# Kernel tuning notes

Hardware: AMD Instinct MI355X
Metric: run time of the kernel (lower is better)

Reference implementation:

```python
import jax, jax.numpy as jnp
import numpy as np

N_HEADS = 16
D_EMBED = 1024
D_CROSS = 768
D_HEAD = D_EMBED // N_HEADS
B, S = 4, 2048


def setup_inputs() -> dict:
    key = jax.random.key(0)
    ks = jax.random.split(key, 10)
    sq = lambda k, shp, fan: jax.random.normal(k, shp, jnp.float32) / np.sqrt(fan)
    return {
        "x": jax.random.normal(ks[0], (B, S, D_EMBED), jnp.float32),
        "y": jax.random.normal(ks[1], (B, S, D_CROSS), jnp.float32),
        "Wq": sq(ks[2], (D_EMBED, D_EMBED), D_EMBED),
        "bq": jnp.zeros((D_EMBED,), jnp.float32),
        "Wk": sq(ks[3], (D_CROSS, D_EMBED), D_CROSS),
        "bk": jnp.zeros((D_EMBED,), jnp.float32),
        "Wv": sq(ks[4], (D_CROSS, D_EMBED), D_CROSS),
        "bv": jnp.zeros((D_EMBED,), jnp.float32),
        "Wo": sq(ks[5], (D_EMBED, D_EMBED), D_EMBED),
        "bo": jnp.zeros((D_EMBED,), jnp.float32),
    }


def reference(x, y, Wq, bq, Wk, bk, Wv, bv, Wo, bo):
    b, s, _ = y.shape
    q = x @ Wq + bq  # [b, s, d_embed]
    k = y @ Wk + bk
    v = y @ Wv + bv
    # [b, h, s, d_head]
    q = q.reshape(b, s, N_HEADS, D_HEAD).transpose(0, 2, 1, 3)
    k = k.reshape(b, s, N_HEADS, D_HEAD).transpose(0, 2, 1, 3)
    v = v.reshape(b, s, N_HEADS, D_HEAD).transpose(0, 2, 1, 3)
    scale = 1.0 / np.sqrt(D_HEAD).astype(np.float32)
    scores = jnp.einsum("bhqd,bhkd->bhqk", q, k) * scale
    weights = jax.nn.softmax(scores, axis=-1)
    out = jnp.einsum("bhqk,bhkd->bhqd", weights, v)
    out = out.transpose(0, 2, 1, 3).reshape(x.shape)
    return out @ Wo + bo
```

## Files before the change

kernel.cpp:

```cpp
#include <hip/hip_runtime.h>

#define NHEADS 16
#define DEMBED 1024
#define DCROSS 768
#define DHEAD  64
#define BATCH  4
#define SLEN   2048
#define MROWS  (BATCH * SLEN)

using bf16   = __bf16;
using bf16x8 = __attribute__((ext_vector_type(8))) __bf16;
using bf16x4 = __attribute__((ext_vector_type(4))) __bf16;
using bf16x2 = __attribute__((ext_vector_type(2))) __bf16;
using f32x4  = __attribute__((ext_vector_type(4))) float;
using f32x16 = __attribute__((ext_vector_type(16))) float;

__device__ __forceinline__ f32x4 mfma_bf16(bf16x8 a, bf16x8 b, f32x4 c) {
    return __builtin_amdgcn_mfma_f32_16x16x32_bf16(a, b, c, 0, 0, 0);
}
__device__ __forceinline__ f32x16 mfma32(bf16x8 a, bf16x8 b, f32x16 c) {
    return __builtin_amdgcn_mfma_f32_32x32x16_bf16(a, b, c, 0, 0, 0);
}

__device__ __forceinline__ void gl2lds16(const void* g, void* l) {
    __builtin_amdgcn_global_load_lds(
        (const __attribute__((address_space(1))) void*)g,
        (__attribute__((address_space(3))) void*)l, 16, 0, 0);
}

struct PrepArgs {
    const float* wsrc[4]; bf16* wdst[4]; int wK[4];
    const float *x, *y; bf16 *xb, *yb;
};
#define NTRB 4096
__global__ void prep_all(PrepArgs a) {
    const int bid = blockIdx.x;
    const int tid = threadIdx.x;
    if (bid < NTRB) {
        __shared__ float tile[32][33];
        const int which = bid >> 10, rem = bid & 1023;
        const int K = a.wK[which], N = DEMBED;
        const int n0 = (rem & 31) * 32, k0 = (rem >> 5) * 32;
        if (k0 >= K) return;
        const float* W = a.wsrc[which];
        bf16* Wt = a.wdst[which];
        const int tx = tid & 31, ty = tid >> 5;
#pragma unroll
        for (int i = 0; i < 32; i += 8)
            tile[ty + i][tx] = W[(size_t)(k0 + ty + i) * N + n0 + tx];
        __syncthreads();
#pragma unroll
        for (int i = 0; i < 32; i += 8)
            Wt[(size_t)(n0 + ty + i) * K + k0 + tx] = (bf16)tile[tx][ty + i];
    } else {
        const int n4x = MROWS * DEMBED / 4;
        const int n4y = MROWS * DCROSS / 4;
        int i = (bid - NTRB) * 256 + tid;
        const float* src; bf16* dst; int j;
        if (i < n4x) { src = a.x; dst = a.xb; j = i; }
        else { j = i - n4x; if (j >= n4y) return; src = a.y; dst = a.yb; }
        float4 v = ((const float4*)src)[j];
        bf16x4 o = { (bf16)v.x, (bf16)v.y, (bf16)v.z, (bf16)v.w };
        ((bf16x4*)dst)[j] = o;
    }
}

struct QkvArgs {
    const bf16 *xb, *yb, *Wqt, *Wkt, *Wvt;
    const float *bq, *bk, *bv;
    bf16 *Qb, *Kb, *Vt;
    float qscale;
};
__global__ __launch_bounds__(256, 3) void gemm_qkv(QkvArgs a) {
    __shared__ bf16 As[128 * 64];
    __shared__ bf16 Bs[128 * 64];
    const int id = blockIdx.x;
    const int cls = id >> 9;
    const bf16 *A, *Bt;
    const float* bias;
    int K, m0, n0;
    if (cls == 0) { int t = id;        m0 = (t >> 3) * 128; n0 = (t & 7) * 128;
                    A = a.xb;  Bt = a.Wqt; bias = a.bq; K = DEMBED; }
    else if (cls == 1) { int t = id - 512;  m0 = (t >> 3) * 128; n0 = (t & 7) * 128;
                    A = a.yb;  Bt = a.Wkt; bias = a.bk; K = DCROSS; }
    else { int t = id - 1024; m0 = (t >> 6) * 128; n0 = (t & 63) * 128;
                    A = a.Wvt; Bt = a.yb;  bias = a.bv; K = DCROSS; }

    const int tid  = threadIdx.x;
    const int wave = tid >> 6, lane = tid & 63;
    const int quad = lane >> 4, l15 = lane & 15;
    const int wr = wave >> 1, wc = wave & 1;

    const int srow = wave * 8 + (lane >> 3);
    const int scol = ((lane & 7) ^ (lane >> 3)) * 8;
    char* ldsA0 = (char*)As + wave * 1024;
    char* ldsB0 = (char*)Bs + wave * 1024;
    const bf16* gA0 = A + (size_t)(m0 + srow) * K + scol;
    const bf16* gB0 = Bt + (size_t)(n0 + srow) * K + scol;

    const int sw = l15 & 7;

    f32x4 acc[4][4] = {};

    for (int kt = 0; kt < K; kt += 64) {
        __syncthreads();
#pragma unroll
        for (int c = 0; c < 4; c++)
            gl2lds16(gA0 + (size_t)c * 32 * K + kt, ldsA0 + c * 4096);
#pragma unroll
        for (int c = 0; c < 4; c++)
            gl2lds16(gB0 + (size_t)c * 32 * K + kt, ldsB0 + c * 4096);
        __syncthreads();

#pragma unroll
        for (int kg = 0; kg < 2; kg++) {
            bf16x8 af[4], bfr[4];
#pragma unroll
            for (int i = 0; i < 4; i++)
                af[i] = *(const bf16x8*)((const char*)As +
                         (wr * 64 + i * 16 + l15) * 128 + (((kg * 4 + quad) ^ sw) * 16));
#pragma unroll
            for (int i = 0; i < 4; i++)
                bfr[i] = *(const bf16x8*)((const char*)Bs +
                         (wc * 64 + i * 16 + l15) * 128 + (((kg * 4 + quad) ^ sw) * 16));
#pragma unroll
            for (int fr = 0; fr < 4; fr++)
#pragma unroll
                for (int fc = 0; fc < 4; fc++)
                    acc[fr][fc] = mfma_bf16(af[fr], bfr[fc], acc[fr][fc]);
        }
    }

    if (cls < 2) {
        bf16* Cout = (cls == 0) ? a.Qb : a.Kb;
        const float alpha = (cls == 0) ? a.qscale : 1.0f;
#pragma unroll
        for (int fr = 0; fr < 4; fr++) {
            int row = m0 + wr * 64 + fr * 16 + quad * 4;
#pragma unroll
            for (int fc = 0; fc < 4; fc++) {
                int col = n0 + wc * 64 + fc * 16 + l15;
                float bv = bias[col];
#pragma unroll
                for (int r = 0; r < 4; r++)
                    Cout[(size_t)(row + r) * DEMBED + col] =
                        (bf16)((acc[fr][fc][r] + bv) * alpha);
            }
        }
    } else {
        const int b = n0 >> 11;
        const size_t bbase = (size_t)b * DEMBED * SLEN;
#pragma unroll
        for (int fr = 0; fr < 4; fr++) {
            int row = m0 + wr * 64 + fr * 16 + quad * 4;
#pragma unroll
            for (int fc = 0; fc < 4; fc++) {
                int col = n0 + wc * 64 + fc * 16 + l15;
                int s = col & (SLEN - 1);
#pragma unroll
                for (int r = 0; r < 4; r++)
                    a.Vt[bbase + (size_t)(row + r) * SLEN + s] =
                        (bf16)(acc[fr][fc][r] + bias[row + r]);
            }
        }
    }
}

__global__ __launch_bounds__(256, 3) void gemm_o(const bf16* __restrict__ A,
                                                 const bf16* __restrict__ Bt,
                                                 const float* __restrict__ bias,
                                                 float* __restrict__ Cout) {
    const int K = DEMBED, N = DEMBED;
    __shared__ bf16 As[128 * 64];
    __shared__ bf16 Bs[128 * 64];
    const int tid  = threadIdx.x;
    const int wave = tid >> 6, lane = tid & 63;
    const int quad = lane >> 4, l15 = lane & 15;
    const int m0 = blockIdx.x * 128, n0 = blockIdx.y * 128;
    const int wr = wave >> 1, wc = wave & 1;

    const int srow = wave * 8 + (lane >> 3);
    const int scol = ((lane & 7) ^ (lane >> 3)) * 8;
    char* ldsA0 = (char*)As + wave * 1024;
    char* ldsB0 = (char*)Bs + wave * 1024;
    const bf16* gA0 = A + (size_t)(m0 + srow) * K + scol;
    const bf16* gB0 = Bt + (size_t)(n0 + srow) * K + scol;

    const int sw = l15 & 7;

    f32x4 acc[4][4] = {};

    for (int kt = 0; kt < K; kt += 64) {
        __syncthreads();
#pragma unroll
        for (int c = 0; c < 4; c++)
            gl2lds16(gA0 + (size_t)c * 32 * K + kt, ldsA0 + c * 4096);
#pragma unroll
        for (int c = 0; c < 4; c++)
            gl2lds16(gB0 + (size_t)c * 32 * K + kt, ldsB0 + c * 4096);
        __syncthreads();

#pragma unroll
        for (int kg = 0; kg < 2; kg++) {
            bf16x8 af[4], bfr[4];
#pragma unroll
            for (int i = 0; i < 4; i++)
                af[i] = *(const bf16x8*)((const char*)As +
                         (wr * 64 + i * 16 + l15) * 128 + (((kg * 4 + quad) ^ sw) * 16));
#pragma unroll
            for (int i = 0; i < 4; i++)
                bfr[i] = *(const bf16x8*)((const char*)Bs +
                         (wc * 64 + i * 16 + l15) * 128 + (((kg * 4 + quad) ^ sw) * 16));
#pragma unroll
            for (int fr = 0; fr < 4; fr++)
#pragma unroll
                for (int fc = 0; fc < 4; fc++)
                    acc[fr][fc] = mfma_bf16(af[fr], bfr[fc], acc[fr][fc]);
        }
    }

#pragma unroll
    for (int fr = 0; fr < 4; fr++) {
        int row = m0 + wr * 64 + fr * 16 + quad * 4;
#pragma unroll
        for (int fc = 0; fc < 4; fc++) {
            int col = n0 + wc * 64 + fc * 16 + l15;
            float bv = bias[col];
#pragma unroll
            for (int r = 0; r < 4; r++)
                Cout[(size_t)(row + r) * N + col] = acc[fr][fc][r] + bv;
        }
    }
}

__global__ __launch_bounds__(256, 4) void attn(const bf16* __restrict__ Q,
                                               const bf16* __restrict__ K,
                                               const bf16* __restrict__ Vt,
                                               bf16* __restrict__ O) {
    __shared__ bf16 KsA[2][64 * 64];
    __shared__ bf16 VsA[2][64 * 64];

    const int tid  = threadIdx.x;
    const int wave = tid >> 6, lane = tid & 63;
    const int l31  = lane & 31, H = lane >> 5;
    const int bh = blockIdx.x, b = bh >> 4, h = bh & 15;
    const size_t rowbase = (size_t)b * SLEN;
    const int qb = blockIdx.y * 128 + wave * 32;
    const int hc = h * DHEAD;

    bf16x8 qf[4];
#pragma unroll
    for (int ks = 0; ks < 4; ks++)
        qf[ks] = *(const bf16x8*)(Q + (rowbase + qb + l31) * DEMBED
                                  + hc + ks * 16 + H * 8);

    f32x16 o[2] = {};
    float lsv = 0.0f;

    const bf16* Kbase = K + rowbase * DEMBED + hc;
    const bf16* Vbase = Vt + (size_t)bh * DHEAD * SLEN;

    const int xcol = (((tid & 7) ^ ((tid >> 3) & 7)) * 8);
    const bf16* gK = Kbase + (size_t)(tid >> 3) * DEMBED + xcol;
    const bf16* gV = Vbase + (size_t)(tid >> 3) * SLEN + xcol;

    const int swz = l31 & 7;

    const int off = (bh * 5 + blockIdx.y * 11) & 31;

    auto STAGE = [&](int buf, int kb) {
        char* lk = (char*)KsA + buf * 8192 + wave * 1024;
        char* lv = (char*)VsA + buf * 8192 + wave * 1024;
        gl2lds16(gK + (size_t)kb * DEMBED, lk);
        gl2lds16(gK + (size_t)(kb + 32) * DEMBED, lk + 32 * 128);
        gl2lds16(gV + kb, lv);
        gl2lds16(gV + 32 * SLEN + kb, lv + 32 * 128);
    };

    STAGE(0, off << 6);
    __syncthreads();

    int cur = 0;
    for (int ss = 0; ss < 32; ++ss) {
        if (ss < 31) STAGE(cur ^ 1, ((ss + off + 1) & 31) << 6);

        const char* Kbuf = (const char*)KsA + cur * 8192;
        const char* Vbuf = (const char*)VsA + cur * 8192;

        f32x16 s0 = {}, s1 = {};
#pragma unroll
        for (int ks = 0; ks < 4; ks++) {
            bf16x8 kf0 = *(const bf16x8*)(Kbuf + l31 * 128
                          + (((2 * ks + H) ^ swz) * 16));
            bf16x8 kf1 = *(const bf16x8*)(Kbuf + (32 + l31) * 128
                          + (((2 * ks + H) ^ swz) * 16));
            s0 = mfma32(kf0, qf[ks], s0);
            s1 = mfma32(kf1, qf[ks], s1);
        }

        int c0[8], c1[8];
#pragma unroll
        for (int t = 0; t < 8; t++) {
            float a0 = __builtin_amdgcn_exp2f(s0[2 * t]);
            float a1 = __builtin_amdgcn_exp2f(s0[2 * t + 1]);
            float b0 = __builtin_amdgcn_exp2f(s1[2 * t]);
            float b1 = __builtin_amdgcn_exp2f(s1[2 * t + 1]);
            lsv += (a0 + a1) + (b0 + b1);
            union { bf16x2 h; int i; } p0, p1;
            p0.h[0] = (bf16)a0; p0.h[1] = (bf16)a1;
            p1.h[0] = (bf16)b0; p1.h[1] = (bf16)b1;
            c0[t] = p0.i;
            c1[t] = p1.i;
        }

#pragma unroll
        for (int ks = 0; ks < 4; ks++) {
            const int* cc = (ks < 2) ? c0 : c1;
            const int ksl = ks & 1;
            auto w0 = __builtin_amdgcn_permlane32_swap(cc[4 * ksl + 0],
                                                       cc[4 * ksl + 2], false, false);
            auto w1 = __builtin_amdgcn_permlane32_swap(cc[4 * ksl + 1],
                                                       cc[4 * ksl + 3], false, false);
            union { int i[4]; bf16x8 v; } ap;
            ap.i[0] = w0[0]; ap.i[1] = w1[0]; ap.i[2] = w0[1]; ap.i[3] = w1[1];
#pragma unroll
            for (int dg = 0; dg < 2; dg++) {
                bf16x8 vf = *(const bf16x8*)(Vbuf + (dg * 32 + l31) * 128
                              + (((2 * ks + H) ^ swz) * 16));
                o[dg] = mfma32(ap.v, vf, o[dg]);
            }
        }

        __syncthreads();
        cur ^= 1;
    }

    lsv += __shfl_xor(lsv, 32);
    float inv = 1.0f / lsv;
#pragma unroll
    for (int r = 0; r < 16; r++) {
        const int ql = (r & 3) + 8 * (r >> 2) + 4 * H;
        float iv = __shfl(inv, ql);
#pragma unroll
        for (int dg = 0; dg < 2; dg++)
            O[(rowbase + qb + ql) * DEMBED + hc + dg * 32 + l31] =
                (bf16)(o[dg][r] * iv);
    }
}

extern "C" void kernel_launch(void* const* d_in, const int* in_sizes, int n_in,
                              void* d_out, int out_size, void* d_ws, size_t ws_size,
                              hipStream_t stream) {
    const float* x  = (const float*)d_in[0];
    const float* y  = (const float*)d_in[1];
    const float* Wq = (const float*)d_in[2];
    const float* bq = (const float*)d_in[3];
    const float* Wk = (const float*)d_in[4];
    const float* bk = (const float*)d_in[5];
    const float* Wv = (const float*)d_in[6];
    const float* bv = (const float*)d_in[7];
    const float* Wo = (const float*)d_in[8];
    const float* bo = (const float*)d_in[9];
    float* out = (float*)d_out;

    char* ws = (char*)d_ws;
    size_t off = 0;
    auto alloc = [&](size_t bytes) {
        void* p = ws + off;
        off += (bytes + 255) & ~(size_t)255;
        return p;
    };
    bf16* xb  = (bf16*)alloc((size_t)MROWS * DEMBED * 2);
    bf16* yb  = (bf16*)alloc((size_t)MROWS * DCROSS * 2);
    bf16* Wqt = (bf16*)alloc((size_t)DEMBED * DEMBED * 2);
    bf16* Wkt = (bf16*)alloc((size_t)DEMBED * DCROSS * 2);
    bf16* Wvt = (bf16*)alloc((size_t)DEMBED * DCROSS * 2);
    bf16* Wot = (bf16*)alloc((size_t)DEMBED * DEMBED * 2);
    bf16* Qb  = (bf16*)alloc((size_t)MROWS * DEMBED * 2);
    bf16* Kb  = (bf16*)alloc((size_t)MROWS * DEMBED * 2);
    bf16* Vtb = (bf16*)alloc((size_t)MROWS * DEMBED * 2);
    bf16* Ab  = (bf16*)alloc((size_t)MROWS * DEMBED * 2);
    if (off > ws_size) return;

    {
        PrepArgs a;
        a.wsrc[0] = Wq; a.wdst[0] = Wqt; a.wK[0] = DEMBED;
        a.wsrc[1] = Wk; a.wdst[1] = Wkt; a.wK[1] = DCROSS;
        a.wsrc[2] = Wv; a.wdst[2] = Wvt; a.wK[2] = DCROSS;
        a.wsrc[3] = Wo; a.wdst[3] = Wot; a.wK[3] = DEMBED;
        a.x = x; a.y = y; a.xb = xb; a.yb = yb;
        int ncvt = (MROWS * DEMBED / 4 + MROWS * DCROSS / 4 + 255) / 256;
        prep_all<<<NTRB + ncvt, 256, 0, stream>>>(a);
    }

    {
        QkvArgs a;
        a.xb = xb; a.yb = yb; a.Wqt = Wqt; a.Wkt = Wkt; a.Wvt = Wvt;
        a.bq = bq; a.bk = bk; a.bv = bv;
        a.Qb = Qb; a.Kb = Kb; a.Vt = Vtb;
        a.qscale = 0.125f * 1.4426950408889634f;
        gemm_qkv<<<1536, 256, 0, stream>>>(a);
    }

    attn<<<dim3(BATCH * NHEADS, SLEN / 128), 256, 0, stream>>>(Qb, Kb, Vtb, Ab);

    gemm_o<<<dim3(MROWS / 128, DEMBED / 128), 256, 0, stream>>>(Ab, Wot, bo, out);
}
```

Baseline: 282.6 us.

## Fuse K and V projections into one block sharing the y tile

```diff
diff --git a/kernel.cpp b/kernel.cpp
--- a/kernel.cpp
+++ b/kernel.cpp
@@ -71,21 +71,12 @@
     bf16 *Qb, *Kb, *Vt;
     float qscale;
 };
-__global__ __launch_bounds__(256, 3) void gemm_qkv(QkvArgs a) {
-    __shared__ bf16 As[128 * 64];
-    __shared__ bf16 Bs[128 * 64];
+__global__ __launch_bounds__(256, 2) void gemm_qkv(QkvArgs a) {
+    __shared__ bf16 Ys[128 * 64];
+    __shared__ bf16 Ks[128 * 64];
+    __shared__ bf16 Vs[128 * 64];
+
     const int id = blockIdx.x;
-    const int cls = id >> 9;
-    const bf16 *A, *Bt;
-    const float* bias;
-    int K, m0, n0;
-    if (cls == 0) { int t = id;        m0 = (t >> 3) * 128; n0 = (t & 7) * 128;
-                    A = a.xb;  Bt = a.Wqt; bias = a.bq; K = DEMBED; }
-    else if (cls == 1) { int t = id - 512;  m0 = (t >> 3) * 128; n0 = (t & 7) * 128;
-                    A = a.yb;  Bt = a.Wkt; bias = a.bk; K = DCROSS; }
-    else { int t = id - 1024; m0 = (t >> 6) * 128; n0 = (t & 63) * 128;
-                    A = a.Wvt; Bt = a.yb;  bias = a.bv; K = DCROSS; }
-
     const int tid  = threadIdx.x;
     const int wave = tid >> 6, lane = tid & 63;
     const int quad = lane >> 4, l15 = lane & 15;
@@ -93,74 +84,144 @@
 
     const int srow = wave * 8 + (lane >> 3);
     const int scol = ((lane & 7) ^ (lane >> 3)) * 8;
-    char* ldsA0 = (char*)As + wave * 1024;
-    char* ldsB0 = (char*)Bs + wave * 1024;
-    const bf16* gA0 = A + (size_t)(m0 + srow) * K + scol;
-    const bf16* gB0 = Bt + (size_t)(n0 + srow) * K + scol;
-
+    char* ldsY0 = (char*)Ys + wave * 1024;
+    char* ldsK0 = (char*)Ks + wave * 1024;
+    char* ldsV0 = (char*)Vs + wave * 1024;
     const int sw = l15 & 7;
 
-    f32x4 acc[4][4] = {};
-
-    for (int kt = 0; kt < K; kt += 64) {
-        __syncthreads();
-#pragma unroll
-        for (int c = 0; c < 4; c++)
-            gl2lds16(gA0 + (size_t)c * 32 * K + kt, ldsA0 + c * 4096);
-#pragma unroll
-        for (int c = 0; c < 4; c++)
-            gl2lds16(gB0 + (size_t)c * 32 * K + kt, ldsB0 + c * 4096);
-        __syncthreads();
-
-#pragma unroll
-        for (int kg = 0; kg < 2; kg++) {
-            bf16x8 af[4], bfr[4];
-#pragma unroll
-            for (int i = 0; i < 4; i++)
-                af[i] = *(const bf16x8*)((const char*)As +
-                         (wr * 64 + i * 16 + l15) * 128 + (((kg * 4 + quad) ^ sw) * 16));
-#pragma unroll
-            for (int i = 0; i < 4; i++)
-                bfr[i] = *(const bf16x8*)((const char*)Bs +
-                         (wc * 64 + i * 16 + l15) * 128 + (((kg * 4 + quad) ^ sw) * 16));
-#pragma unroll
-            for (int fr = 0; fr < 4; fr++)
-#pragma unroll
-                for (int fc = 0; fc < 4; fc++)
-                    acc[fr][fc] = mfma_bf16(af[fr], bfr[fc], acc[fr][fc]);
-        }
-    }
-
-    if (cls < 2) {
-        bf16* Cout = (cls == 0) ? a.Qb : a.Kb;
-        const float alpha = (cls == 0) ? a.qscale : 1.0f;
+    if (id < 512) {
+        const int t = id;
+        const int m0 = (t >> 3) * 128, n0 = (t & 7) * 128;
+        const int K = DEMBED;
+        const bf16* gA0 = a.xb + (size_t)(m0 + srow) * K + scol;
+        const bf16* gB0 = a.Wqt + (size_t)(n0 + srow) * K + scol;
+
+        f32x4 acc[4][4] = {};
+
+        for (int kt = 0; kt < K; kt += 64) {
+            __syncthreads();
+#pragma unroll
+            for (int c = 0; c < 4; c++)
+                gl2lds16(gA0 + (size_t)c * 32 * K + kt, ldsY0 + c * 4096);
+#pragma unroll
+            for (int c = 0; c < 4; c++)
+                gl2lds16(gB0 + (size_t)c * 32 * K + kt, ldsK0 + c * 4096);
+            __syncthreads();
+
+#pragma unroll
+            for (int kg = 0; kg < 2; kg++) {
+                bf16x8 af[4], bfr[4];
+#pragma unroll
+                for (int i = 0; i < 4; i++)
+                    af[i] = *(const bf16x8*)((const char*)Ys +
+                             (wr * 64 + i * 16 + l15) * 128 + (((kg * 4 + quad) ^ sw) * 16));
+#pragma unroll
+                for (int i = 0; i < 4; i++)
+                    bfr[i] = *(const bf16x8*)((const char*)Ks +
+                             (wc * 64 + i * 16 + l15) * 128 + (((kg * 4 + quad) ^ sw) * 16));
+#pragma unroll
+                for (int fr = 0; fr < 4; fr++)
+#pragma unroll
+                    for (int fc = 0; fc < 4; fc++)
+                        acc[fr][fc] = mfma_bf16(af[fr], bfr[fc], acc[fr][fc]);
+            }
+        }
+
+        const float alpha = a.qscale;
 #pragma unroll
         for (int fr = 0; fr < 4; fr++) {
             int row = m0 + wr * 64 + fr * 16 + quad * 4;
 #pragma unroll
             for (int fc = 0; fc < 4; fc++) {
                 int col = n0 + wc * 64 + fc * 16 + l15;
-                float bv = bias[col];
+                float bv = a.bq[col];
 #pragma unroll
                 for (int r = 0; r < 4; r++)
-                    Cout[(size_t)(row + r) * DEMBED + col] =
+                    a.Qb[(size_t)(row + r) * DEMBED + col] =
                         (bf16)((acc[fr][fc][r] + bv) * alpha);
             }
         }
     } else {
-        const int b = n0 >> 11;
-        const size_t bbase = (size_t)b * DEMBED * SLEN;
+        const int t = id - 512;
+        const int m0 = (t >> 3) * 128;
+        const int n0 = (t & 7) * 128;
+        const int K = DCROSS;
+        const bf16* gY = a.yb  + (size_t)(m0 + srow) * K + scol;
+        const bf16* gK = a.Wkt + (size_t)(n0 + srow) * K + scol;
+        const bf16* gV = a.Wvt + (size_t)(n0 + srow) * K + scol;
+
+        f32x4 accK[4][4] = {};
+        f32x4 accV[4][4] = {};
+
+        for (int kt = 0; kt < K; kt += 64) {
+            __syncthreads();
+#pragma unroll
+            for (int c = 0; c < 4; c++)
+                gl2lds16(gY + (size_t)c * 32 * K + kt, ldsY0 + c * 4096);
+#pragma unroll
+            for (int c = 0; c < 4; c++)
+                gl2lds16(gK + (size_t)c * 32 * K + kt, ldsK0 + c * 4096);
+#pragma unroll
+            for (int c = 0; c < 4; c++)
+                gl2lds16(gV + (size_t)c * 32 * K + kt, ldsV0 + c * 4096);
+            __syncthreads();
+
+#pragma unroll
+            for (int kg = 0; kg < 2; kg++) {
+                bf16x8 yf[4], kf[4], vf[4];
+#pragma unroll
+                for (int i = 0; i < 4; i++)
+                    yf[i] = *(const bf16x8*)((const char*)Ys +
+                             (wr * 64 + i * 16 + l15) * 128 + (((kg * 4 + quad) ^ sw) * 16));
+#pragma unroll
+                for (int i = 0; i < 4; i++)
+                    kf[i] = *(const bf16x8*)((const char*)Ks +
+                             (wc * 64 + i * 16 + l15) * 128 + (((kg * 4 + quad) ^ sw) * 16));
+#pragma unroll
+                for (int i = 0; i < 4; i++)
+                    vf[i] = *(const bf16x8*)((const char*)Vs +
+                             (wc * 64 + i * 16 + l15) * 128 + (((kg * 4 + quad) ^ sw) * 16));
+                __builtin_amdgcn_s_setprio(1);
+#pragma unroll
+                for (int fr = 0; fr < 4; fr++)
+#pragma unroll
+                    for (int fc = 0; fc < 4; fc++)
+                        accK[fr][fc] = mfma_bf16(yf[fr], kf[fc], accK[fr][fc]);
+#pragma unroll
+                for (int fr = 0; fr < 4; fr++)
+#pragma unroll
+                    for (int fc = 0; fc < 4; fc++)
+                        accV[fr][fc] = mfma_bf16(vf[fr], yf[fc], accV[fr][fc]);
+                __builtin_amdgcn_s_setprio(0);
+            }
+        }
+
 #pragma unroll
         for (int fr = 0; fr < 4; fr++) {
             int row = m0 + wr * 64 + fr * 16 + quad * 4;
 #pragma unroll
             for (int fc = 0; fc < 4; fc++) {
                 int col = n0 + wc * 64 + fc * 16 + l15;
-                int s = col & (SLEN - 1);
+                float bv = a.bk[col];
 #pragma unroll
                 for (int r = 0; r < 4; r++)
-                    a.Vt[bbase + (size_t)(row + r) * SLEN + s] =
-                        (bf16)(acc[fr][fc][r] + bias[row + r]);
+                    a.Kb[(size_t)(row + r) * DEMBED + col] =
+                        (bf16)(accK[fr][fc][r] + bv);
+            }
+        }
+        const int b = m0 >> 11;
+        const size_t bbase = (size_t)b * DEMBED * SLEN;
+#pragma unroll
+        for (int fr = 0; fr < 4; fr++) {
+            int row_v = n0 + wc * 64 + fr * 16 + quad * 4;
+#pragma unroll
+            for (int fc = 0; fc < 4; fc++) {
+                int col_v = m0 + wr * 64 + fc * 16 + l15;
+                int s = col_v & (SLEN - 1);
+#pragma unroll
+                for (int r = 0; r < 4; r++)
+                    a.Vt[bbase + (size_t)(row_v + r) * SLEN + s] =
+                        (bf16)(accV[fr][fc][r] + a.bv[row_v + r]);
             }
         }
     }
@@ -399,7 +460,7 @@
         a.bq = bq; a.bk = bk; a.bv = bv;
         a.Qb = Qb; a.Kb = Kb; a.Vt = Vtb;
         a.qscale = 0.125f * 1.4426950408889634f;
-        gemm_qkv<<<1536, 256, 0, stream>>>(a);
+        gemm_qkv<<<1024, 256, 0, stream>>>(a);
     }
 
     attn<<<dim3(BATCH * NHEADS, SLEN / 128), 256, 0, stream>>>(Qb, Kb, Vtb, Ab);
```

Measured after the change: 280.6 us. About the same (-0.7%).
